# Performance work log

Measured on AMD Instinct MI355X. Metric: run time of the kernel, lower is better.

## Reference

```python
import jax, jax.numpy as jnp
import numpy as np

BIT_DEPTH = 8  # feature squeezing

def setup_inputs() -> dict:
    key = jax.random.key(0)
    ks = jax.random.split(key, 8)
    B, C, H, W = 8, 256, 64, 64
    Cq = C // 8
    x = jax.random.normal(ks[0], (B, C, H, W), dtype=jnp.float32)
    # 1x1 conv weights stored as [out, in] (kernel dims squeezed)
    wq = jax.random.normal(ks[1], (Cq, C), dtype=jnp.float32) * 0.05
    bq = jax.random.normal(ks[2], (Cq,), dtype=jnp.float32) * 0.05
    wk = jax.random.normal(ks[3], (Cq, C), dtype=jnp.float32) * 0.05
    bk = jax.random.normal(ks[4], (Cq,), dtype=jnp.float32) * 0.05
    wv = jax.random.normal(ks[5], (C, C), dtype=jnp.float32) * 0.05
    bv = jax.random.normal(ks[6], (C,), dtype=jnp.float32) * 0.05
    gamma = jax.random.normal(ks[7], (1,), dtype=jnp.float32) * 0.1
    return {"x": x, "wq": wq, "bq": bq, "wk": wk, "bk": bk, "wv": wv, "bv": bv, "gamma": gamma}

def reference(x, wq, bq, wk, bk, wv, bv, gamma):
    B, C, H, W = x.shape
    N = H * W
    xf = x.reshape(B, C, N)  # flatten spatial
    # 1x1 convs == per-pixel linear projections
    q = jnp.einsum('bcn,oc->bon', xf, wq) + bq[None, :, None]   # [B, C/8, N]
    k = jnp.einsum('bcn,oc->bon', xf, wk) + bk[None, :, None]   # [B, C/8, N]
    v = jnp.einsum('bcn,oc->bon', xf, wv) + bv[None, :, None]   # [B, C, N]
    energy = jnp.einsum('bcn,bcm->bnm', q, k)                   # [B, N, N] (no scaling, as in source)
    attn = jax.nn.softmax(energy, axis=-1)
    out = jnp.einsum('bcm,bnm->bcn', v, attn).reshape(B, C, H, W)
    out = gamma[0] * out + out               # gamma-scaled residual of attention output
    scale = jnp.float32(2 ** BIT_DEPTH)
    return jnp.floor(out * scale) / scale    # feature squeezing (bit_depth=8)
```

## Files before the change

kernel.cpp:

```cpp
#include <hip/hip_runtime.h>
#include <math.h>

namespace {
constexpr int BB = 8;
constexpr int CH = 256;
constexpr int CQ = 32;
constexpr int NN = 4096;
}

typedef float f32x4 __attribute__((ext_vector_type(4)));
typedef short bf16x8 __attribute__((ext_vector_type(8)));
typedef unsigned short us8 __attribute__((ext_vector_type(8)));

#define MFMA16(a, b, c) __builtin_amdgcn_mfma_f32_16x16x32_bf16(a, b, c, 0, 0, 0)

__device__ __forceinline__ unsigned short f2bf(float x) {
    unsigned int u = __float_as_uint(x);
    u += 0x7fffu + ((u >> 16) & 1u);
    return (unsigned short)(u >> 16);
}
__device__ __forceinline__ float bf2f(unsigned short h) {
    return __uint_as_float(((unsigned int)h) << 16);
}
__device__ __forceinline__ void gload16(const void* g, void* l) {
    __builtin_amdgcn_global_load_lds(
        (const __attribute__((address_space(1))) unsigned int*)g,
        (__attribute__((address_space(3))) unsigned int*)l, 16, 0, 0);
}

__global__ __launch_bounds__(256) void wsplit_kernel(
    const float* __restrict__ wq, const float* __restrict__ wk,
    const float* __restrict__ wv,
    unsigned short* __restrict__ wh, unsigned short* __restrict__ wl)
{
    int idx = blockIdx.x * 256 + threadIdx.x;
    float v;
    if (idx < 8192)       v = wq[idx];
    else if (idx < 16384) v = wk[idx - 8192];
    else                  v = wv[idx - 16384];
    unsigned short hi = f2bf(v);
    wh[idx] = hi;
    wl[idx] = f2bf(v - bf2f(hi));
}

__global__ __launch_bounds__(256) void transpose_kernel(
    const float* __restrict__ x,
    unsigned short* __restrict__ xh, unsigned short* __restrict__ xl)
{
    __shared__ float xf[64 * 68];
    __shared__ unsigned short hs[64 * 80];
    __shared__ unsigned short ls[64 * 80];
    const int t  = threadIdx.x;
    const int b  = blockIdx.x >> 8;
    const int tl = blockIdx.x & 255;
    const int c0 = (tl >> 6) * 64;
    const int n0 = (tl & 63) * 64;

    #pragma unroll
    for (int i = 0; i < 4; ++i) {
        int idx = i * 256 + t;
        int c = idx >> 4, nf = idx & 15;
        float4 v4 = *(const float4*)(x + ((size_t)(b * 256 + c0 + c)) * NN + n0 + nf * 4);
        *(float4*)(xf + c * 68 + nf * 4) = v4;
    }
    __syncthreads();

    const int n = t & 63;
    #pragma unroll
    for (int loop = 0; loop < 2; ++loop) {
        int chunk = (t >> 6) + 4 * loop;
        us8 h8, l8;
        #pragma unroll
        for (int j = 0; j < 8; ++j) {
            float v = xf[(chunk * 8 + j) * 68 + n];
            unsigned short hi = f2bf(v);
            h8[j] = hi;
            l8[j] = f2bf(v - bf2f(hi));
        }
        *(us8*)(hs + n * 80 + chunk * 8) = h8;
        *(us8*)(ls + n * 80 + chunk * 8) = l8;
    }
    __syncthreads();

    {
        int rn = t >> 2, piece = t & 3;
        size_t grow = ((size_t)(b * NN + n0 + rn)) * 256 + c0 + piece * 16;
        *(f32x4*)((float*)0 + 0);
        *(us8*)(xh + grow)     = *(const us8*)(hs + rn * 80 + piece * 16);
        *(us8*)(xh + grow + 8) = *(const us8*)(hs + rn * 80 + piece * 16 + 8);
        *(us8*)(xl + grow)     = *(const us8*)(ls + rn * 80 + piece * 16);
        *(us8*)(xl + grow + 8) = *(const us8*)(ls + rn * 80 + piece * 16 + 8);
    }
}

#define PJ_XL 32768
#define PJ_VE 16384
__global__ __launch_bounds__(256, 2) void proj_kernel(
    const unsigned short* __restrict__ xh, const unsigned short* __restrict__ xl,
    const unsigned short* __restrict__ wh, const unsigned short* __restrict__ wl,
    const float* __restrict__ bq, const float* __restrict__ bk,
    const float* __restrict__ bv,
    unsigned short* __restrict__ qh, unsigned short* __restrict__ ql,
    unsigned short* __restrict__ kh, unsigned short* __restrict__ kl,
    unsigned short* __restrict__ vt)
{
    __shared__ __align__(16) unsigned char smem[65536];
    const int t    = threadIdx.x;
    const int lane = t & 63;
    const int w    = t >> 6;
    const int l16  = lane & 15;
    const int quad = lane >> 4;
    const int b    = blockIdx.x >> 6;
    const int n0   = (blockIdx.x & 63) << 6;

    const unsigned char* xhB = (const unsigned char*)(xh + ((size_t)b * NN + n0) * 256);
    const unsigned char* xlB = (const unsigned char*)(xl + ((size_t)b * NN + n0) * 256);
    #pragma unroll
    for (int j = 0; j < 8; ++j) {
        int idx = j * 256 + t;
        int r = idx >> 5, cl = idx & 31;
        int cg = cl ^ (r & 7);
        gload16(xhB + (size_t)r * 512 + cg * 16, smem + idx * 16);
        gload16(xlB + (size_t)r * 512 + cg * 16, smem + PJ_XL + idx * 16);
    }
    __syncthreads();

    f32x4 acc[5][4] = {};
    #pragma unroll 1
    for (int kc = 0; kc < 8; ++kc) {
        bf16x8 ah[5], al[5];
        #pragma unroll
        for (int i = 0; i < 5; ++i) {
            int och = (w * 5 + i) * 16 + l16;
            ah[i] = *(const bf16x8*)(wh + och * 256 + kc * 32 + quad * 8);
            al[i] = *(const bf16x8*)(wl + och * 256 + kc * 32 + quad * 8);
        }
        #pragma unroll
        for (int nt = 0; nt < 4; ++nt) {
            int roff = (nt * 16 + l16) * 512 + (((kc * 4 + quad) ^ (l16 & 7)) * 16);
            bf16x8 bh = *(const bf16x8*)(smem + roff);
            bf16x8 bl = *(const bf16x8*)(smem + PJ_XL + roff);
            #pragma unroll
            for (int i = 0; i < 5; ++i) {
                acc[i][nt] = MFMA16(ah[i], bh, acc[i][nt]);
                acc[i][nt] = MFMA16(al[i], bh, acc[i][nt]);
                acc[i][nt] = MFMA16(ah[i], bl, acc[i][nt]);
            }
        }
    }
    __syncthreads();

    #pragma unroll
    for (int i = 0; i < 5; ++i) {
        int tile = w * 5 + i;
        if (tile < 4) {
            #pragma unroll
            for (int r = 0; r < 4; ++r) {
                int och = tile * 16 + quad * 4 + r;
                float bias = (och < 32) ? bq[och] : bk[och - 32];
                int arr = (och < 32) ? 0 : 2;
                int oq = och & 31;
                #pragma unroll
                for (int nt = 0; nt < 4; ++nt) {
                    float val = acc[i][nt][r] + bias;
                    unsigned short hi = f2bf(val);
                    unsigned short lo = f2bf(val - bf2f(hi));
                    *(unsigned short*)(smem + arr * 4096 + (nt * 16 + l16) * 64 + oq * 2) = hi;
                    *(unsigned short*)(smem + (arr + 1) * 4096 + (nt * 16 + l16) * 64 + oq * 2) = lo;
                }
            }
        } else {
            #pragma unroll
            for (int r = 0; r < 4; ++r) {
                int voch = tile * 16 + quad * 4 + r - 64;
                float bias = bv[voch];
                #pragma unroll
                for (int nt = 0; nt < 4; ++nt) {
                    *(unsigned short*)(smem + PJ_VE + voch * 136 + (nt * 16 + l16) * 2)
                        = f2bf(acc[i][nt][r] + bias);
                }
            }
        }
    }
    __syncthreads();

    {
        unsigned short* dsts[4] = { qh, ql, kh, kl };
        int arr = t >> 6, n = t & 63;
        unsigned short* dst = dsts[arr] + ((size_t)b * NN + n0 + n) * 32;
        #pragma unroll
        for (int i = 0; i < 4; ++i)
            *(us8*)(dst + i * 8) = *(const us8*)(smem + arr * 4096 + n * 64 + i * 16);
    }
    #pragma unroll
    for (int p = 0; p < 4; ++p) {
        int voch = p * 64 + (t >> 2), piece = t & 3;
        unsigned short* dst = vt + ((size_t)b * CH + voch) * NN + n0 + piece * 16;
        *(us8*)(dst)     = *(const us8*)(smem + PJ_VE + voch * 136 + piece * 32);
        *(us8*)(dst + 8) = *(const us8*)(smem + PJ_VE + voch * 136 + piece * 32 + 16);
    }
}

#define A_KH 0
#define A_KL 4096
#define A_V  8192
#define A_P  40960
#define A_SM 50176

__global__ __launch_bounds__(256, 2) void attn_kernel(
    const unsigned short* __restrict__ qh, const unsigned short* __restrict__ ql,
    const unsigned short* __restrict__ kh, const unsigned short* __restrict__ kl,
    const unsigned short* __restrict__ vt, const float* __restrict__ gptr,
    float* __restrict__ out)
{
    __shared__ __align__(16) unsigned char smem[51200];
    const int t    = threadIdx.x;
    const int lane = t & 63;
    const int w    = t >> 6;
    const int l16  = lane & 15;
    const int quad = lane >> 4;
    const int b    = blockIdx.x & 7;
    const int n0   = (blockIdx.x >> 3) << 6;

    bf16x8 qhA[4], qlA[4];
    #pragma unroll
    for (int qt = 0; qt < 4; ++qt) {
        size_t row = (size_t)b * NN + n0 + qt * 16 + l16;
        qhA[qt] = *(const bf16x8*)(qh + row * 32 + quad * 8);
        qlA[qt] = *(const bf16x8*)(ql + row * 32 + quad * 8);
    }

    const unsigned char* khB = (const unsigned char*)(kh + (size_t)b * NN * 32);
    const unsigned char* klB = (const unsigned char*)(kl + (size_t)b * NN * 32);
    const unsigned char* vtB = (const unsigned char*)(vt + (size_t)b * CH * NN);

    f32x4 acc[4][4] = {};
    float S[4][4] = {};

    #pragma unroll 1
    for (int tile = 0; tile < 64; ++tile) {
        const int m0 = tile * 64;
        __syncthreads();
        {
            int r = t >> 2, cl = t & 3;
            int cg = cl ^ ((r >> 1) & 3);
            gload16(khB + (size_t)(m0 + r) * 64 + cg * 16, smem + A_KH + t * 16);
            gload16(klB + (size_t)(m0 + r) * 64 + cg * 16, smem + A_KL + t * 16);
        }
        #pragma unroll
        for (int j = 0; j < 8; ++j) {
            int idx = j * 256 + t;
            int r = idx >> 3, cl = idx & 7;
            int cg = cl ^ (r & 7);
            gload16(vtB + (size_t)r * 8192 + (size_t)m0 * 2 + cg * 16,
                    smem + A_V + idx * 16);
        }
        __syncthreads();

        {
            int row = w * 16 + l16;
            int koff = row * 64 + ((quad ^ ((l16 >> 1) & 3)) * 16);
            bf16x8 bh = *(const bf16x8*)(smem + A_KH + koff);
            bf16x8 bl = *(const bf16x8*)(smem + A_KL + koff);
            #pragma unroll
            for (int qt = 0; qt < 4; ++qt) {
                f32x4 e = { 0.f, 0.f, 0.f, 0.f };
                e = MFMA16(qhA[qt], bh, e);
                e = MFMA16(qlA[qt], bh, e);
                e = MFMA16(qhA[qt], bl, e);
                #pragma unroll
                for (int r = 0; r < 4; ++r) {
                    float p = __expf(e[r]);
                    unsigned short pb = f2bf(p);
                    S[qt][r] += bf2f(pb);
                    *(unsigned short*)(smem + A_P + (qt * 16 + quad * 4 + r) * 144
                                            + (w * 16 + l16) * 2) = pb;
                }
            }
        }
        __syncthreads();

        #pragma unroll
        for (int ks = 0; ks < 2; ++ks) {
            bf16x8 af[4], bfr[4];
            #pragma unroll
            for (int qt = 0; qt < 4; ++qt)
                af[qt] = *(const bf16x8*)(smem + A_P + (qt * 16 + l16) * 144
                                               + ks * 64 + quad * 16);
            #pragma unroll
            for (int ct = 0; ct < 4; ++ct) {
                int row = w * 64 + ct * 16 + l16;
                int ch = (ks * 4 + quad) ^ (l16 & 7);
                bfr[ct] = *(const bf16x8*)(smem + A_V + row * 128 + ch * 16);
            }
            #pragma unroll
            for (int qt = 0; qt < 4; ++qt)
                #pragma unroll
                for (int ct = 0; ct < 4; ++ct)
                    acc[qt][ct] = MFMA16(af[qt], bfr[ct], acc[qt][ct]);
        }
    }

    #pragma unroll
    for (int mask = 1; mask <= 8; mask <<= 1)
        #pragma unroll
        for (int qt = 0; qt < 4; ++qt)
            #pragma unroll
            for (int r = 0; r < 4; ++r)
                S[qt][r] += __shfl_xor(S[qt][r], mask);
    float* SM = (float*)(smem + A_SM);
    if (l16 == 0) {
        #pragma unroll
        for (int qt = 0; qt < 4; ++qt)
            #pragma unroll
            for (int r = 0; r < 4; ++r)
                SM[w * 64 + qt * 16 + quad * 4 + r] = S[qt][r];
    }
    __syncthreads();

    const float g1 = 1.f + gptr[0];
    float* ob = out + (size_t)b * CH * NN;
    #pragma unroll
    for (int qt = 0; qt < 4; ++qt) {
        float is[4];
        #pragma unroll
        for (int r = 0; r < 4; ++r) {
            int qi = qt * 16 + quad * 4 + r;
            float Sf = SM[qi] + SM[64 + qi] + SM[128 + qi] + SM[192 + qi];
            is[r] = g1 / Sf;
        }
        #pragma unroll
        for (int ct = 0; ct < 4; ++ct) {
            float4 o4;
            o4.x = floorf(acc[qt][ct][0] * is[0] * 256.f) * 0.00390625f;
            o4.y = floorf(acc[qt][ct][1] * is[1] * 256.f) * 0.00390625f;
            o4.z = floorf(acc[qt][ct][2] * is[2] * 256.f) * 0.00390625f;
            o4.w = floorf(acc[qt][ct][3] * is[3] * 256.f) * 0.00390625f;
            *(float4*)(ob + (size_t)(w * 64 + ct * 16 + l16) * NN
                          + n0 + qt * 16 + quad * 4) = o4;
        }
    }
}

extern "C" void kernel_launch(void* const* d_in, const int* in_sizes, int n_in,
                              void* d_out, int out_size, void* d_ws, size_t ws_size,
                              hipStream_t stream) {
    const float* x  = (const float*)d_in[0];
    const float* wq = (const float*)d_in[1];
    const float* bq = (const float*)d_in[2];
    const float* wk = (const float*)d_in[3];
    const float* bk = (const float*)d_in[4];
    const float* wv = (const float*)d_in[5];
    const float* bv = (const float*)d_in[6];
    const float* gm = (const float*)d_in[7];
    float* out = (float*)d_out;

    unsigned short* ws = (unsigned short*)d_ws;
    const size_t XSZ = (size_t)BB * NN * 256;
    const size_t WSZ = 320 * 256;
    const size_t QSZ = (size_t)BB * NN * 32;
    unsigned short* xh = ws;
    unsigned short* xl = xh + XSZ;
    unsigned short* wh = xl + XSZ;
    unsigned short* wl = wh + WSZ;
    unsigned short* qh = wl + WSZ;
    unsigned short* ql = qh + QSZ;
    unsigned short* kh = ql + QSZ;
    unsigned short* kl = kh + QSZ;
    unsigned short* vt = kl + QSZ;

    wsplit_kernel<<<320, 256, 0, stream>>>(wq, wk, wv, wh, wl);
    transpose_kernel<<<2048, 256, 0, stream>>>(x, xh, xl);
    proj_kernel<<<512, 256, 0, stream>>>(xh, xl, wh, wl, bq, bk, bv,
                                         qh, ql, kh, kl, vt);
    attn_kernel<<<512, 256, 0, stream>>>(qh, ql, kh, kl, vt, gm, out);
}
```

Baseline: 247.7 us.

## Load K and V fragments directly into registers and double-buffer P in LDS

The attention loop stops staging K and V tiles through shared memory. Each lane now loads its MFMA fragments straight from global memory into registers, and the next K fragment is prefetched one tile ahead. The probability tile is double-buffered in LDS, which removes two of the three barriers per tile and shrinks shared memory from about 51KB to 19KB. In exchange, V loads are issued in the same tile they are used, so their global latency may be exposed, and register pressure rises. A stray null-pointer expression in the conversion kernel is also removed.

```diff
diff --git a/kernel.cpp b/kernel.cpp
--- a/kernel.cpp
+++ b/kernel.cpp
@@ -85,7 +85,6 @@
     {
         int rn = t >> 2, piece = t & 3;
         size_t grow = ((size_t)(b * NN + n0 + rn)) * 256 + c0 + piece * 16;
-        *(f32x4*)((float*)0 + 0);
         *(us8*)(xh + grow)     = *(const us8*)(hs + rn * 80 + piece * 16);
         *(us8*)(xh + grow + 8) = *(const us8*)(hs + rn * 80 + piece * 16 + 8);
         *(us8*)(xl + grow)     = *(const us8*)(ls + rn * 80 + piece * 16);
@@ -201,11 +200,9 @@
     }
 }
 
-#define A_KH 0
-#define A_KL 4096
-#define A_V  8192
-#define A_P  40960
-#define A_SM 50176
+#define A_P0 0
+#define A_P1 9216
+#define A_SM 18432
 
 __global__ __launch_bounds__(256, 2) void attn_kernel(
     const unsigned short* __restrict__ qh, const unsigned short* __restrict__ ql,
@@ -213,7 +210,7 @@
     const unsigned short* __restrict__ vt, const float* __restrict__ gptr,
     float* __restrict__ out)
 {
-    __shared__ __align__(16) unsigned char smem[51200];
+    __shared__ __align__(16) unsigned char smem[19456];
     const int t    = threadIdx.x;
     const int lane = t & 63;
     const int w    = t >> 6;
@@ -230,75 +227,69 @@
         qlA[qt] = *(const bf16x8*)(ql + row * 32 + quad * 8);
     }
 
-    const unsigned char* khB = (const unsigned char*)(kh + (size_t)b * NN * 32);
-    const unsigned char* klB = (const unsigned char*)(kl + (size_t)b * NN * 32);
-    const unsigned char* vtB = (const unsigned char*)(vt + (size_t)b * CH * NN);
+    const unsigned short* vbase[4];
+    #pragma unroll
+    for (int ct = 0; ct < 4; ++ct)
+        vbase[ct] = vt + (size_t)b * CH * NN
+                       + (size_t)(w * 64 + ct * 16 + l16) * NN + quad * 8;
+    const unsigned short* khbase = kh + ((size_t)b * NN + w * 16 + l16) * 32 + quad * 8;
+    const unsigned short* klbase = kl + ((size_t)b * NN + w * 16 + l16) * 32 + quad * 8;
 
     f32x4 acc[4][4] = {};
     float S[4][4] = {};
+
+    bf16x8 kch = *(const bf16x8*)(khbase);
+    bf16x8 kcl = *(const bf16x8*)(klbase);
 
     #pragma unroll 1
     for (int tile = 0; tile < 64; ++tile) {
         const int m0 = tile * 64;
+        const int m1 = ((tile + 1) & 63) * 64;
+
+        bf16x8 vr0[4], vr1[4];
+        #pragma unroll
+        for (int ct = 0; ct < 4; ++ct) {
+            vr0[ct] = *(const bf16x8*)(vbase[ct] + m0);
+            vr1[ct] = *(const bf16x8*)(vbase[ct] + m0 + 32);
+        }
+        bf16x8 knh = *(const bf16x8*)(khbase + (size_t)m1 * 32);
+        bf16x8 knl = *(const bf16x8*)(klbase + (size_t)m1 * 32);
+
+        unsigned char* P = smem + ((tile & 1) ? A_P1 : A_P0);
+        #pragma unroll
+        for (int qt = 0; qt < 4; ++qt) {
+            f32x4 e = { 0.f, 0.f, 0.f, 0.f };
+            e = MFMA16(qhA[qt], kch, e);
+            e = MFMA16(qlA[qt], kch, e);
+            e = MFMA16(qhA[qt], kcl, e);
+            #pragma unroll
+            for (int r = 0; r < 4; ++r) {
+                float p = __expf(e[r]);
+                unsigned short pb = f2bf(p);
+                S[qt][r] += bf2f(pb);
+                *(unsigned short*)(P + (qt * 16 + quad * 4 + r) * 144
+                                     + (w * 16 + l16) * 2) = pb;
+            }
+        }
         __syncthreads();
-        {
-            int r = t >> 2, cl = t & 3;
-            int cg = cl ^ ((r >> 1) & 3);
-            gload16(khB + (size_t)(m0 + r) * 64 + cg * 16, smem + A_KH + t * 16);
-            gload16(klB + (size_t)(m0 + r) * 64 + cg * 16, smem + A_KL + t * 16);
-        }
-        #pragma unroll
-        for (int j = 0; j < 8; ++j) {
-            int idx = j * 256 + t;
-            int r = idx >> 3, cl = idx & 7;
-            int cg = cl ^ (r & 7);
-            gload16(vtB + (size_t)r * 8192 + (size_t)m0 * 2 + cg * 16,
-                    smem + A_V + idx * 16);
-        }
-        __syncthreads();
-
-        {
-            int row = w * 16 + l16;
-            int koff = row * 64 + ((quad ^ ((l16 >> 1) & 3)) * 16);
-            bf16x8 bh = *(const bf16x8*)(smem + A_KH + koff);
-            bf16x8 bl = *(const bf16x8*)(smem + A_KL + koff);
+
+        #pragma unroll
+        for (int ks = 0; ks < 2; ++ks) {
+            bf16x8 af[4];
+            #pragma unroll
+            for (int qt = 0; qt < 4; ++qt)
+                af[qt] = *(const bf16x8*)(P + (qt * 16 + l16) * 144
+                                            + ks * 64 + quad * 16);
             #pragma unroll
             for (int qt = 0; qt < 4; ++qt) {
-                f32x4 e = { 0.f, 0.f, 0.f, 0.f };
-                e = MFMA16(qhA[qt], bh, e);
-                e = MFMA16(qlA[qt], bh, e);
-                e = MFMA16(qhA[qt], bl, e);
-                #pragma unroll
-                for (int r = 0; r < 4; ++r) {
-                    float p = __expf(e[r]);
-                    unsigned short pb = f2bf(p);
-                    S[qt][r] += bf2f(pb);
-                    *(unsigned short*)(smem + A_P + (qt * 16 + quad * 4 + r) * 144
-                                            + (w * 16 + l16) * 2) = pb;
-                }
-            }
-        }
-        __syncthreads();
-
-        #pragma unroll
-        for (int ks = 0; ks < 2; ++ks) {
-            bf16x8 af[4], bfr[4];
-            #pragma unroll
-            for (int qt = 0; qt < 4; ++qt)
-                af[qt] = *(const bf16x8*)(smem + A_P + (qt * 16 + l16) * 144
-                                               + ks * 64 + quad * 16);
-            #pragma unroll
-            for (int ct = 0; ct < 4; ++ct) {
-                int row = w * 64 + ct * 16 + l16;
-                int ch = (ks * 4 + quad) ^ (l16 & 7);
-                bfr[ct] = *(const bf16x8*)(smem + A_V + row * 128 + ch * 16);
-            }
-            #pragma unroll
-            for (int qt = 0; qt < 4; ++qt)
                 #pragma unroll
                 for (int ct = 0; ct < 4; ++ct)
-                    acc[qt][ct] = MFMA16(af[qt], bfr[ct], acc[qt][ct]);
-        }
+                    acc[qt][ct] = MFMA16(af[qt], ks ? vr1[ct] : vr0[ct],
+                                         acc[qt][ct]);
+            }
+        }
+        kch = knh;
+        kcl = knl;
     }
 
     #pragma unroll
```

New measurement: 268.8 us. 1.08x slower.
